# Kernel tuning notes

Measured on AMD Instinct MI355X. Metric: run time of the kernel, lower is better.

## Reference

```python
import jax, jax.numpy as jnp
import numpy as np

B, N = 16, 1023            # batch, signal length
T = N + 1                  # frames: hop=1, gaussian centers 0..N
F_BINS = N + 1             # rfft(2N) -> N+1 frequency bins
HID, NCLS = 128, 10


def setup_inputs() -> dict:
    key = jax.random.key(0)
    k = jax.random.split(key, 3)
    x = jax.random.normal(k[0], (B, N), dtype=jnp.float32)
    lambd = jnp.asarray(32.0, dtype=jnp.float32)  # learnable window width (sigma)
    feat = F_BINS * T
    W1 = jax.random.normal(k[1], (HID, feat), dtype=jnp.float32) / np.float32(np.sqrt(feat))
    b1 = jnp.zeros((HID,), jnp.float32)
    W2 = jax.random.normal(k[2], (NCLS, HID), dtype=jnp.float32) / np.float32(np.sqrt(HID))
    b2 = jnp.zeros((NCLS,), jnp.float32)
    return {"x": x, "lambd": lambd, "W1": W1, "b1": b1, "W2": W2, "b2": b2}


def _spectrogram(x, lambd):
    """Whole-signal differentiable Gaussian spectrogram (non-optimized path, hop=1).

    S[b, f, t] = | sum_n (x[b,n]-mean) * exp(-0.5*((n-t)/|lambd|)^2) * e^{-2pi i f n / (2N)} |^2
    Vectorized over the batch (replaces the per-sample Python loop).
    """
    n = x.shape[-1]
    sigma = jnp.abs(lambd)
    t = jnp.arange(n, dtype=jnp.float32)
    tc = jnp.arange(n + 1, dtype=jnp.float32)  # frame centers 0..n (n//hop + 1 frames)
    win = jnp.exp(-0.5 * ((t[None, :] - tc[:, None]) / sigma) ** 2)  # [T, n]
    xc = x - jnp.mean(x, axis=-1, keepdims=True)                     # per-sample mean removal
    xw = xc[:, None, :] * win[None]                                  # [B, T, n]
    spec = jnp.abs(jnp.fft.rfft(xw, n=2 * n, axis=-1)) ** 2          # [B, T, n+1]
    return jnp.transpose(spec, (0, 2, 1))[:, None]                   # [B, 1, n+1, T]


def reference(x, lambd, W1, b1, W2, b2):
    s = _spectrogram(x, lambd)                       # [B, 1, F_BINS, T]
    flat = s.reshape(s.shape[0], -1)                 # [B, F_BINS*T]
    h = jax.nn.relu(flat @ W1.T + b1)                # fc1 + relu
    out = h @ W2.T + b2                              # fc2
    return out, s
```

## Files before the change

### kernel.cpp

```cpp
#include <hip/hip_runtime.h>
#include <math.h>

#define NSIG   1023
#define BATCH  16
#define FT     1024
#define KW     256
#define RHALF  128
#define XPAD   1280
#define HID    128

#define OFF_XCP  0u
#define OFF_G    20480u
#define OFF_HRAW 20736u
#define OFF_TAB  22784u
#define TAB_ECH  0u
#define TAB_ECL  262144u
#define TAB_ESH  524288u
#define TAB_ESL  786432u

typedef int    i32x4  __attribute__((ext_vector_type(4)));
typedef float  f32x4  __attribute__((ext_vector_type(4)));
typedef __bf16 bf16x8 __attribute__((ext_vector_type(8)));
typedef unsigned short u16;

static __device__ __forceinline__ unsigned bfbits(float v) {
    unsigned u = __builtin_bit_cast(unsigned, v);
    return (u + 0x7fffu + ((u >> 16) & 1u)) >> 16;
}

__global__ void k_prep(const float* __restrict__ x, float* __restrict__ ws) {
    int b = blockIdx.x;
    __shared__ float red[256];
    float s = 0.f;
    for (int i = threadIdx.x; i < NSIG; i += 256) s += x[b * NSIG + i];
    red[threadIdx.x] = s;
    __syncthreads();
    for (int o = 128; o > 0; o >>= 1) {
        if (threadIdx.x < o) red[threadIdx.x] += red[threadIdx.x + o];
        __syncthreads();
    }
    float mean = red[0] * (1.0f / NSIG);
    float* xcp = ws + OFF_XCP + b * XPAD;
    for (int i = threadIdx.x; i < XPAD; i += 256) {
        int n = i - RHALF;
        xcp[i] = (n >= 0 && n < NSIG) ? (x[b * NSIG + n] - mean) : 0.f;
    }
}

__global__ void k_tables(const float* __restrict__ lambd, float* __restrict__ ws) {
    int bid = blockIdx.x;
    if (bid == 1024) {
        float sigma = fabsf(lambd[0]);
        float inv2s2 = 0.5f / (sigma * sigma);
        for (int i = threadIdx.x; i < KW; i += 256) {
            float d = (float)(i - RHALF);
            ws[OFF_G + i] = expf(-d * d * inv2s2);
        }
        for (int i = threadIdx.x; i < 2048; i += 256) ws[OFF_HRAW + i] = 0.f;
        return;
    }
    int idx = bid * 256 + threadIdx.x;
    int f = idx >> 8, k = idx & 255;
    int d = k - RHALF;
    int p = f * d;
    int m = p % 2046; if (m < 0) m += 2046;
    double ang = (double)m * (6.283185307179586476925286766559 / 2046.0);
    double sv, cv;
    sincos(ang, &sv, &cv);
    float cf = (float)cv, sf = (float)sv;
    u16* tab = (u16*)(ws + OFF_TAB);
    unsigned chb = bfbits(cf);
    float chf = __builtin_bit_cast(float, chb << 16);
    unsigned clb = bfbits(cf - chf);
    unsigned shb = bfbits(sf);
    float shf = __builtin_bit_cast(float, shb << 16);
    unsigned slb = bfbits(sf - shf);
    tab[TAB_ECH + idx] = (u16)chb;
    tab[TAB_ECL + idx] = (u16)clb;
    tab[TAB_ESH + idx] = (u16)shb;
    tab[TAB_ESL + idx] = (u16)slb;
}

__global__ __launch_bounds__(512, 4) void k_spec(const float* __restrict__ ws,
                                                 float* __restrict__ out) {
    __shared__ u16 yH[64 * 256];
    __shared__ u16 yL[64 * 256];
    int t0 = blockIdx.x * 64, f0 = blockIdx.y * 128, b = blockIdx.z;
    int tid = threadIdx.x;
    int wave = tid >> 6, lane = tid & 63;
    int lo = lane & 15, hi4 = lane >> 4;
    const u16* tab = (const u16*)(ws + OFF_TAB);
    const float* xcp = ws + OFF_XCP + b * XPAD;
    const float* gw  = ws + OFF_G;

    #pragma unroll
    for (int i = 0; i < 4; i++) {
        int idx = tid + i * 512;
        int t = idx >> 5, kg = idx & 31;
        int k = kg * 8;
        const float* xp = xcp + t0 + t + k;
        float4 g0 = *(const float4*)&gw[k];
        float4 g1 = *(const float4*)&gw[k + 4];
        float yv[8];
        yv[0] = xp[0] * g0.x; yv[1] = xp[1] * g0.y;
        yv[2] = xp[2] * g0.z; yv[3] = xp[3] * g0.w;
        yv[4] = xp[4] * g1.x; yv[5] = xp[5] * g1.y;
        yv[6] = xp[6] * g1.z; yv[7] = xp[7] * g1.w;
        unsigned hb[8], lb[8];
        #pragma unroll
        for (int j = 0; j < 8; j++) {
            unsigned u = __builtin_bit_cast(unsigned, yv[j]);
            unsigned h = (u + 0x7fffu + ((u >> 16) & 1u)) & 0xffff0000u;
            float hf = __builtin_bit_cast(float, h);
            hb[j] = h >> 16;
            lb[j] = bfbits(yv[j] - hf);
        }
        i32x4 ph, pl;
        ph.x = (int)(hb[0] | (hb[1] << 16)); ph.y = (int)(hb[2] | (hb[3] << 16));
        ph.z = (int)(hb[4] | (hb[5] << 16)); ph.w = (int)(hb[6] | (hb[7] << 16));
        pl.x = (int)(lb[0] | (lb[1] << 16)); pl.y = (int)(lb[2] | (lb[3] << 16));
        pl.z = (int)(lb[4] | (lb[5] << 16)); pl.w = (int)(lb[6] | (lb[7] << 16));
        int wb = ((t * 512 + kg * 16) ^ ((t & 7) << 4));
        *(i32x4*)((char*)yH + wb) = ph;
        *(i32x4*)((char*)yL + wb) = pl;
    }
    __syncthreads();

    size_t arow = (size_t)(f0 + wave * 16 + lo) * 256 + hi4 * 8;
    const u16* pech = tab + TAB_ECH + arow;
    const u16* pecl = tab + TAB_ECL + arow;
    const u16* pesh = tab + TAB_ESH + arow;
    const u16* pesl = tab + TAB_ESL + arow;

    f32x4 reA[4], imA[4];
    #pragma unroll
    for (int i = 0; i < 4; i++) {
        reA[i] = (f32x4){0.f, 0.f, 0.f, 0.f};
        imA[i] = (f32x4){0.f, 0.f, 0.f, 0.f};
    }

    #pragma unroll 2
    for (int c = 0; c < 8; c++) {
        i32x4 ech = *(const i32x4*)(pech + c * 32);
        i32x4 ecl = *(const i32x4*)(pecl + c * 32);
        i32x4 esh = *(const i32x4*)(pesh + c * 32);
        i32x4 esl = *(const i32x4*)(pesl + c * 32);
        #pragma unroll
        for (int tt = 0; tt < 4; tt++) {
            int tr = tt * 16 + lo;
            int rb = ((tr * 512 + c * 64 + hi4 * 16) ^ ((tr & 7) << 4));
            i32x4 yh = *(const i32x4*)((const char*)yH + rb);
            i32x4 yl = *(const i32x4*)((const char*)yL + rb);
            asm("v_mfma_f32_16x16x32_bf16 %0, %1, %2, %0" : "+v"(reA[tt]) : "v"(ech), "v"(yh));
            asm("v_mfma_f32_16x16x32_bf16 %0, %1, %2, %0" : "+v"(imA[tt]) : "v"(esh), "v"(yh));
            asm("v_mfma_f32_16x16x32_bf16 %0, %1, %2, %0" : "+v"(reA[tt]) : "v"(ech), "v"(yl));
            asm("v_mfma_f32_16x16x32_bf16 %0, %1, %2, %0" : "+v"(imA[tt]) : "v"(esh), "v"(yl));
            asm("v_mfma_f32_16x16x32_bf16 %0, %1, %2, %0" : "+v"(reA[tt]) : "v"(ecl), "v"(yh));
            asm("v_mfma_f32_16x16x32_bf16 %0, %1, %2, %0" : "+v"(imA[tt]) : "v"(esl), "v"(yh));
        }
    }
    asm volatile("s_nop 7\n\ts_nop 7");

    float* dS = out + 160;
    #pragma unroll
    for (int tt = 0; tt < 4; tt++) {
        #pragma unroll
        for (int r = 0; r < 4; r++) {
            int f = f0 + wave * 16 + hi4 * 4 + r;
            float re = reA[tt][r], im = imA[tt][r];
            dS[((size_t)b << 20) + (size_t)f * 1024 + t0 + tt * 16 + lo] = re * re + im * im;
        }
    }
}

static __device__ __forceinline__ bf16x8 packc4(float4 a, float4 b) {
    bf16x8 r;
    r[0] = (__bf16)a.x; r[1] = (__bf16)a.y; r[2] = (__bf16)a.z; r[3] = (__bf16)a.w;
    r[4] = (__bf16)b.x; r[5] = (__bf16)b.y; r[6] = (__bf16)b.z; r[7] = (__bf16)b.w;
    return r;
}
static __device__ __forceinline__ bf16x8 packcv(f32x4 a, f32x4 b) {
    bf16x8 r;
    r[0] = (__bf16)a.x; r[1] = (__bf16)a.y; r[2] = (__bf16)a.z; r[3] = (__bf16)a.w;
    r[4] = (__bf16)b.x; r[5] = (__bf16)b.y; r[6] = (__bf16)b.z; r[7] = (__bf16)b.w;
    return r;
}

static __device__ __forceinline__ void stageW(const float* base, float* dst,
                                              int rowLane, int colb0) {
    #pragma unroll
    for (int i = 0; i < 8; i++) {
        int sw = ((2 * (i & 3)) + rowLane) << 4;
        const float* src = base + (size_t)(2 * i + rowLane) * (1u << 20)
                         + ((colb0 ^ sw) >> 2);
        __builtin_amdgcn_global_load_lds(
            (const __attribute__((address_space(1))) void*)src,
            (__attribute__((address_space(3))) void*)((char*)dst + i * 1024),
            16, 0, 0);
    }
}

__global__ __launch_bounds__(256, 2) void k_fc1(const float* __restrict__ S,
                                                const float* __restrict__ W1,
                                                float* __restrict__ hraw) {
    __shared__ float Wl[4][2][2048];
    int tid = threadIdx.x;
    int wave = tid >> 6, lane = tid & 63;
    int bq = lane >> 4, lo = lane & 15;
    int ks = (blockIdx.x << 2) | wave;
    size_t kb = (size_t)ks * 512;

    int rowLane = lane >> 5;
    int colb0 = (lane & 31) << 4;
    int sw = (lo & 7) << 4;

    const float* Sp = S + ((size_t)lo << 20) + kb + bq * 8;
    float* buf0 = &Wl[wave][0][0];
    float* buf1 = &Wl[wave][1][0];

    bf16x8 af[4][4];
    #pragma unroll
    for (int s = 0; s < 4; s++) {
        #pragma unroll
        for (int q = 0; q < 4; q++) {
            float4 a0 = *(const float4*)(Sp + s * 128 + q * 32);
            float4 a1 = *(const float4*)(Sp + s * 128 + q * 32 + 4);
            af[s][q] = packc4(a0, a1);
        }
    }

    f32x4 acc[8];
    #pragma unroll
    for (int j = 0; j < 8; j++) acc[j] = (f32x4){0.f, 0.f, 0.f, 0.f};

    stageW(W1 + kb, buf0, rowLane, colb0);

    #pragma unroll
    for (int c = 0; c < 32; c++) {
        const int jt = c >> 2, s = c & 3;
        if (c < 31) {
            const int cn = c + 1, jn = cn >> 2, sn = cn & 3;
            stageW(W1 + ((size_t)(jn * 16) << 20) + kb + sn * 128,
                   (c & 1) ? buf0 : buf1, rowLane, colb0);
            asm volatile("s_waitcnt vmcnt(8)" ::: "memory");
        } else {
            asm volatile("s_waitcnt vmcnt(0)" ::: "memory");
        }
        const char* wb = (const char*)((c & 1) ? buf1 : buf0);
        #pragma unroll
        for (int q = 0; q < 4; q++) {
            int cb = q * 128 + bq * 32;
            f32x4 w0 = *(const f32x4*)(wb + lo * 512 + (cb ^ sw));
            f32x4 w1 = *(const f32x4*)(wb + lo * 512 + ((cb + 16) ^ sw));
            acc[jt] = __builtin_amdgcn_mfma_f32_16x16x32_bf16(af[s][q], packcv(w0, w1),
                                                              acc[jt], 0, 0, 0);
        }
    }

    float* red = &Wl[wave][0][0];
    #pragma unroll
    for (int jt = 0; jt < 8; jt++) {
        #pragma unroll
        for (int r = 0; r < 4; r++) {
            red[(bq * 4 + r) * 128 + jt * 16 + lo] = acc[jt][r];
        }
    }
    __syncthreads();
    for (int p = tid; p < 2048; p += 256) {
        float v = Wl[0][0][p] + Wl[1][0][p] + Wl[2][0][p] + Wl[3][0][p];
        atomicAdd(&hraw[p], v);
    }
}

__global__ void k_head(const float* __restrict__ hraw, const float* __restrict__ b1,
                       const float* __restrict__ W2, const float* __restrict__ b2,
                       float* __restrict__ out) {
    __shared__ float hl[2048];
    int tid = threadIdx.x;
    for (int p = tid; p < 2048; p += 256) {
        float hv = hraw[p] + b1[p & 127];
        hl[p] = hv > 0.f ? hv : 0.f;
    }
    __syncthreads();
    if (tid < 160) {
        int b = tid / 10, c = tid - b * 10;
        float s = b2[c];
        for (int j = 0; j < 128; j++) s += hl[b * 128 + j] * W2[c * 128 + j];
        out[b * 10 + c] = s;
    }
}

extern "C" void kernel_launch(void* const* d_in, const int* in_sizes, int n_in,
                              void* d_out, int out_size, void* d_ws, size_t ws_size,
                              hipStream_t stream) {
    const float* x     = (const float*)d_in[0];
    const float* lambd = (const float*)d_in[1];
    const float* W1    = (const float*)d_in[2];
    const float* b1    = (const float*)d_in[3];
    const float* W2    = (const float*)d_in[4];
    const float* b2    = (const float*)d_in[5];
    float* out = (float*)d_out;
    float* ws  = (float*)d_ws;

    hipLaunchKernelGGL(k_prep,   dim3(16),         dim3(256), 0, stream, x, ws);
    hipLaunchKernelGGL(k_tables, dim3(1025),       dim3(256), 0, stream, lambd, ws);
    hipLaunchKernelGGL(k_spec,   dim3(16, 8, 16),  dim3(512), 0, stream, ws, out);
    hipLaunchKernelGGL(k_fc1,    dim3(512),        dim3(256), 0, stream,
                       out + 160, W1, ws + OFF_HRAW);
    hipLaunchKernelGGL(k_head,   dim3(1),          dim3(256), 0, stream,
                       ws + OFF_HRAW, b1, W2, b2, out);
}
```

Before: 200.5 us.

## Stage W1 through registers with single LDS buffer and raise occupancy

Replaces the double-buffered global_load_lds staging of W1 with a register prefetch: the next chunk is loaded into registers while the current chunk's MFMAs run, then written to a single swizzled LDS buffer. The loop order becomes s-outer/jt-inner so only four bf16 A fragments are live at a time, loaded when s changes. LDS per block is halved and launch bounds go to 3 blocks per SM, aiming at higher occupancy and memory-latency hiding. In exchange there are extra register-to-LDS store instructions, a full vmcnt(0) wait every iteration, and the reliance on wave-local ordering without barriers when reusing the single buffer.

```diff
diff --git a/kernel.cpp b/kernel.cpp
--- a/kernel.cpp
+++ b/kernel.cpp
@@ -186,78 +186,103 @@
     return r;
 }
 
-static __device__ __forceinline__ void stageW(const float* base, float* dst,
-                                              int rowLane, int colb0) {
-    #pragma unroll
-    for (int i = 0; i < 8; i++) {
-        int sw = ((2 * (i & 3)) + rowLane) << 4;
-        const float* src = base + (size_t)(2 * i + rowLane) * (1u << 20)
-                         + ((colb0 ^ sw) >> 2);
-        __builtin_amdgcn_global_load_lds(
-            (const __attribute__((address_space(1))) void*)src,
-            (__attribute__((address_space(3))) void*)((char*)dst + i * 1024),
-            16, 0, 0);
-    }
-}
-
-__global__ __launch_bounds__(256, 2) void k_fc1(const float* __restrict__ S,
+__global__ __launch_bounds__(256, 3) void k_fc1(const float* __restrict__ S,
                                                 const float* __restrict__ W1,
                                                 float* __restrict__ hraw) {
-    __shared__ float Wl[4][2][2048];
+    __shared__ float Wl[4][2048];
     int tid = threadIdx.x;
     int wave = tid >> 6, lane = tid & 63;
     int bq = lane >> 4, lo = lane & 15;
     int ks = (blockIdx.x << 2) | wave;
     size_t kb = (size_t)ks * 512;
 
-    int rowLane = lane >> 5;
-    int colb0 = (lane & 31) << 4;
+    int lr0 = lane >> 5;
+    int c16 = lane & 31;
     int sw = (lo & 7) << 4;
 
     const float* Sp = S + ((size_t)lo << 20) + kb + bq * 8;
-    float* buf0 = &Wl[wave][0][0];
-    float* buf1 = &Wl[wave][1][0];
-
-    bf16x8 af[4][4];
-    #pragma unroll
-    for (int s = 0; s < 4; s++) {
-        #pragma unroll
-        for (int q = 0; q < 4; q++) {
-            float4 a0 = *(const float4*)(Sp + s * 128 + q * 32);
-            float4 a1 = *(const float4*)(Sp + s * 128 + q * 32 + 4);
-            af[s][q] = packc4(a0, a1);
-        }
-    }
+    float* buf = &Wl[wave][0];
+
+    f32x4 st0, st1, st2, st3, st4, st5, st6, st7;
+    #define LD_CHUNK(JT, SS)                                                     \
+        {                                                                        \
+            const float* _b = W1 + ((size_t)((JT) * 16) << 20) + kb + (SS) * 128;\
+            st0 = *(const f32x4*)(_b + ((size_t)(0  + lr0) << 20) + c16 * 4);    \
+            st1 = *(const f32x4*)(_b + ((size_t)(2  + lr0) << 20) + c16 * 4);    \
+            st2 = *(const f32x4*)(_b + ((size_t)(4  + lr0) << 20) + c16 * 4);    \
+            st3 = *(const f32x4*)(_b + ((size_t)(6  + lr0) << 20) + c16 * 4);    \
+            st4 = *(const f32x4*)(_b + ((size_t)(8  + lr0) << 20) + c16 * 4);    \
+            st5 = *(const f32x4*)(_b + ((size_t)(10 + lr0) << 20) + c16 * 4);    \
+            st6 = *(const f32x4*)(_b + ((size_t)(12 + lr0) << 20) + c16 * 4);    \
+            st7 = *(const f32x4*)(_b + ((size_t)(14 + lr0) << 20) + c16 * 4);    \
+        }
+    #define ST_CHUNK()                                                           \
+        {                                                                        \
+            *(f32x4*)((char*)buf + ((0  + lr0) * 512 + ((c16 * 16) ^ (((0  + lr0) & 7) << 4)))) = st0; \
+            *(f32x4*)((char*)buf + ((2  + lr0) * 512 + ((c16 * 16) ^ (((2  + lr0) & 7) << 4)))) = st1; \
+            *(f32x4*)((char*)buf + ((4  + lr0) * 512 + ((c16 * 16) ^ (((4  + lr0) & 7) << 4)))) = st2; \
+            *(f32x4*)((char*)buf + ((6  + lr0) * 512 + ((c16 * 16) ^ (((6  + lr0) & 7) << 4)))) = st3; \
+            *(f32x4*)((char*)buf + ((8  + lr0) * 512 + ((c16 * 16) ^ (((8  + lr0) & 7) << 4)))) = st4; \
+            *(f32x4*)((char*)buf + ((10 + lr0) * 512 + ((c16 * 16) ^ (((10 + lr0) & 7) << 4)))) = st5; \
+            *(f32x4*)((char*)buf + ((12 + lr0) * 512 + ((c16 * 16) ^ (((12 + lr0) & 7) << 4)))) = st6; \
+            *(f32x4*)((char*)buf + ((14 + lr0) * 512 + ((c16 * 16) ^ (((14 + lr0) & 7) << 4)))) = st7; \
+        }
 
     f32x4 acc[8];
     #pragma unroll
     for (int j = 0; j < 8; j++) acc[j] = (f32x4){0.f, 0.f, 0.f, 0.f};
 
-    stageW(W1 + kb, buf0, rowLane, colb0);
+    LD_CHUNK(0, 0);
+    asm volatile("s_waitcnt vmcnt(0)" ::: "memory");
+    ST_CHUNK();
+
+    bf16x8 af0, af1, af2, af3;
 
     #pragma unroll
     for (int c = 0; c < 32; c++) {
-        const int jt = c >> 2, s = c & 3;
+        const int s = c >> 3, jt = c & 7;
+        if (jt == 0) {
+            const float* sp = Sp + s * 128;
+            float4 a0 = *(const float4*)(sp);
+            float4 a1 = *(const float4*)(sp + 4);
+            float4 a2 = *(const float4*)(sp + 32);
+            float4 a3 = *(const float4*)(sp + 36);
+            float4 a4 = *(const float4*)(sp + 64);
+            float4 a5 = *(const float4*)(sp + 68);
+            float4 a6 = *(const float4*)(sp + 96);
+            float4 a7 = *(const float4*)(sp + 100);
+            af0 = packc4(a0, a1); af1 = packc4(a2, a3);
+            af2 = packc4(a4, a5); af3 = packc4(a6, a7);
+        }
         if (c < 31) {
-            const int cn = c + 1, jn = cn >> 2, sn = cn & 3;
-            stageW(W1 + ((size_t)(jn * 16) << 20) + kb + sn * 128,
-                   (c & 1) ? buf0 : buf1, rowLane, colb0);
-            asm volatile("s_waitcnt vmcnt(8)" ::: "memory");
-        } else {
+            const int cn = c + 1, sn = cn >> 3, jn = cn & 7;
+            LD_CHUNK(jn, sn);
+        }
+        {
+            int cb0 = bq * 32;
+            f32x4 w0 = *(const f32x4*)((char*)buf + lo * 512 + ((cb0      ) ^ sw));
+            f32x4 w1 = *(const f32x4*)((char*)buf + lo * 512 + ((cb0 +  16) ^ sw));
+            acc[jt] = __builtin_amdgcn_mfma_f32_16x16x32_bf16(af0, packcv(w0, w1), acc[jt], 0, 0, 0);
+            f32x4 w2 = *(const f32x4*)((char*)buf + lo * 512 + ((cb0 + 128) ^ sw));
+            f32x4 w3 = *(const f32x4*)((char*)buf + lo * 512 + ((cb0 + 144) ^ sw));
+            acc[jt] = __builtin_amdgcn_mfma_f32_16x16x32_bf16(af1, packcv(w2, w3), acc[jt], 0, 0, 0);
+            f32x4 w4 = *(const f32x4*)((char*)buf + lo * 512 + ((cb0 + 256) ^ sw));
+            f32x4 w5 = *(const f32x4*)((char*)buf + lo * 512 + ((cb0 + 272) ^ sw));
+            acc[jt] = __builtin_amdgcn_mfma_f32_16x16x32_bf16(af2, packcv(w4, w5), acc[jt], 0, 0, 0);
+            f32x4 w6 = *(const f32x4*)((char*)buf + lo * 512 + ((cb0 + 384) ^ sw));
+            f32x4 w7 = *(const f32x4*)((char*)buf + lo * 512 + ((cb0 + 400) ^ sw));
+            acc[jt] = __builtin_amdgcn_mfma_f32_16x16x32_bf16(af3, packcv(w6, w7), acc[jt], 0, 0, 0);
+        }
+        if (c < 31) {
             asm volatile("s_waitcnt vmcnt(0)" ::: "memory");
-        }
-        const char* wb = (const char*)((c & 1) ? buf1 : buf0);
-        #pragma unroll
-        for (int q = 0; q < 4; q++) {
-            int cb = q * 128 + bq * 32;
-            f32x4 w0 = *(const f32x4*)(wb + lo * 512 + (cb ^ sw));
-            f32x4 w1 = *(const f32x4*)(wb + lo * 512 + ((cb + 16) ^ sw));
-            acc[jt] = __builtin_amdgcn_mfma_f32_16x16x32_bf16(af[s][q], packcv(w0, w1),
-                                                              acc[jt], 0, 0, 0);
-        }
-    }
-
-    float* red = &Wl[wave][0][0];
+            ST_CHUNK();
+        }
+    }
+    #undef LD_CHUNK
+    #undef ST_CHUNK
+    asm volatile("s_nop 7\n\ts_nop 7");
+
+    float* red = &Wl[wave][0];
     #pragma unroll
     for (int jt = 0; jt < 8; jt++) {
         #pragma unroll
@@ -267,7 +292,7 @@
     }
     __syncthreads();
     for (int p = tid; p < 2048; p += 256) {
-        float v = Wl[0][0][p] + Wl[1][0][p] + Wl[2][0][p] + Wl[3][0][p];
+        float v = Wl[0][p] + Wl[1][p] + Wl[2][p] + Wl[3][p];
         atomicAdd(&hraw[p], v);
     }
 }
```

Result: no change. 201.7 us (+0.6%).
